# Kernel tuning notes

Measured on AMD Instinct MI355X. Metric: run time of the kernel, lower is better.

## Reference

```python
import jax, jax.numpy as jnp
import numpy as np

N, F, H, C, E = 100000, 128, 64, 16, 1000000


def _prop(x, src, dst, w):
    # gather source features, scale by edge weight, scatter-add to destinations
    msgs = x[src] * w[:, None]  # [E, H]
    return jax.ops.segment_sum(msgs, dst, num_segments=N)


def _gru(x, h, W_ih, W_hh, b_ih, b_hh):
    gi = x @ W_ih.T + b_ih  # [N, 3H]
    gh = h @ W_hh.T + b_hh
    i_r, i_z, i_n = jnp.split(gi, 3, axis=1)
    h_r, h_z, h_n = jnp.split(gh, 3, axis=1)
    r = jax.nn.sigmoid(i_r + h_r)
    z = jax.nn.sigmoid(i_z + h_z)
    n = jnp.tanh(i_n + r * h_n)
    return (1.0 - z) * n + z * h


def setup_inputs() -> dict:
    key = jax.random.key(0)
    ks = jax.random.split(key, 20)
    s = 0.05
    inp = {
        'x': jax.random.normal(ks[0], (N, F), jnp.float32),
        'edge_index': jax.random.randint(ks[1], (2, E), 0, N),
        'edge_weight': jax.random.uniform(ks[2], (E,), jnp.float32),
        'edge_index_re': jax.random.randint(ks[3], (2, E), 0, N),
        'edge_weight_re': jax.random.uniform(ks[4], (E,), jnp.float32),
        'W_first': jax.random.normal(ks[5], (H, F), jnp.float32) * s,
        'b_first': jnp.zeros((H,), jnp.float32),
        'W_con1': jax.random.normal(ks[6], (H, 2 * H), jnp.float32) * s,
        'b_con1': jnp.zeros((H,), jnp.float32),
        'W_con2': jax.random.normal(ks[7], (H, 2 * H), jnp.float32) * s,
        'b_con2': jnp.zeros((H,), jnp.float32),
        'W_lin1': jax.random.normal(ks[8], (H, H), jnp.float32) * s,
        'b_lin1': jnp.zeros((H,), jnp.float32),
        'W_out': jax.random.normal(ks[9], (C, H), jnp.float32) * s,
        'b_out': jnp.zeros((C,), jnp.float32),
        'W_ih': jax.random.normal(ks[10], (3 * H, H), jnp.float32) * s,
        'W_hh': jax.random.normal(ks[11], (3 * H, H), jnp.float32) * s,
        'b_ih': jnp.zeros((3 * H,), jnp.float32),
        'b_hh': jnp.zeros((3 * H,), jnp.float32),
    }
    return inp


def reference(x, edge_index, edge_weight, edge_index_re, edge_weight_re,
              W_first, b_first, W_con1, b_con1, W_con2, b_con2,
              W_lin1, b_lin1, W_out, b_out, W_ih, W_hh, b_ih, b_hh):
    src, dst = edge_index[0], edge_index[1]
    src_r, dst_r = edge_index_re[0], edge_index_re[1]

    x = x @ W_first.T + b_first  # [N, H]; dropout is identity at inference
    h = x

    x1 = _prop(x, src, dst, edge_weight)
    x2 = _prop(x, src_r, dst_r, edge_weight_re)
    x = jnp.concatenate([x1, x2], axis=1) @ W_con1.T + b_con1
    x = _gru(x, h, W_ih, W_hh, b_ih, b_hh)
    x = x @ W_lin1.T + b_lin1

    x1 = _prop(x, src, dst, edge_weight)
    x2 = _prop(x, src_r, dst_r, edge_weight_re)
    x = jnp.concatenate([x1, x2], axis=1) @ W_con2.T + b_con2
    x = _gru(x, h, W_ih, W_hh, b_ih, b_hh)
    x = x @ W_out.T + b_out
    return jax.nn.log_softmax(x, axis=-1)
```

## Files before the change

### kernel.cpp

```cpp
#include <hip/hip_runtime.h>

#define NN 100000
#define FF 128
#define HH 64
#define CC 16
#define EE 1000000
#define NSEG (2*NN)
#define BSH 11
#define BKD  (1 << BSH)
#define NBUK ((NSEG + BKD - 1) / BKD)
#define EPB 4096
#define P1BLK ((2*EE + EPB - 1) / EPB)

typedef __bf16 bf16;
typedef __attribute__((ext_vector_type(8))) __bf16 bf16x8;
typedef __attribute__((ext_vector_type(4))) __bf16 bf16x4;
typedef __attribute__((ext_vector_type(4))) float f32x4;
typedef __attribute__((ext_vector_type(2))) float f32x2;

__device__ __forceinline__ float fsig(float t)  { return 1.0f/(1.0f+__expf(-t)); }
__device__ __forceinline__ float ftanh(float t) { return 1.0f - 2.0f/(__expf(2.0f*t)+1.0f); }

__device__ __forceinline__ unsigned pack_sw(int s, float w) {
    unsigned short u = __builtin_bit_cast(unsigned short, (bf16)w);
    return ((unsigned)s << 15) | (u & 0x7FFFu);
}

__global__ void precomp_kernel(const float* __restrict__ W_ih, const float* __restrict__ b_ih,
                               const float* __restrict__ Wc1,  const float* __restrict__ bc1,
                               const float* __restrict__ Wc2,  const float* __restrict__ bc2,
                               const float* __restrict__ W_hh, const float* __restrict__ W_first,
                               const float* __restrict__ W_lin1, const float* __restrict__ W_out,
                               bf16* __restrict__ W1bf, float* __restrict__ b1,
                               bf16* __restrict__ W2bf, float* __restrict__ b2,
                               bf16* __restrict__ Whbf, bf16* __restrict__ Wfbf,
                               bf16* __restrict__ Wlbf, bf16* __restrict__ Wobf)
{
    int idx = blockIdx.x*blockDim.x + threadIdx.x;
    const int t0 = 192*128;
    const int t1 = t0 + 192;
    const int t2 = t1 + 192*64;
    const int t3 = t2 + 64*128;
    const int t4 = t3 + 64*64;
    const int t5 = t4 + 16*64;
    if (idx < t0) {
        int j = idx >> 7, k = idx & 127;
        float s1 = 0.f, s2 = 0.f;
        for (int m=0; m<64; ++m) {
            float wih = W_ih[j*64+m];
            s1 += wih * Wc1[m*128+k];
            s2 += wih * Wc2[m*128+k];
        }
        W1bf[idx] = (bf16)s1; W2bf[idx] = (bf16)s2;
    } else if (idx < t1) {
        int j = idx - t0;
        float s1 = b_ih[j], s2 = b_ih[j];
        for (int m=0; m<64; ++m) {
            float wih = W_ih[j*64+m];
            s1 += wih * bc1[m];
            s2 += wih * bc2[m];
        }
        b1[j] = s1; b2[j] = s2;
    } else if (idx < t2) {
        int i = idx - t1;  Whbf[i] = (bf16)W_hh[i];
    } else if (idx < t3) {
        int i = idx - t2;  Wfbf[i] = (bf16)W_first[i];
    } else if (idx < t4) {
        int i = idx - t3;  Wlbf[i] = (bf16)W_lin1[i];
    } else if (idx < t5) {
        int i = idx - t4;  Wobf[i] = (bf16)W_out[i];
    }
}


__global__ __launch_bounds__(256) void bucket_count_kernel(const int* __restrict__ ei,
                                                           const int* __restrict__ ei_re,
                                                           int* __restrict__ bkcnt)
{
    __shared__ int hist[NBUK];
    const int t = threadIdx.x;
    for (int i=t; i<NBUK; i+=256) hist[i] = 0;
    __syncthreads();
    const long e0 = (long)blockIdx.x * EPB;
    #pragma unroll
    for (int it=0; it<16; ++it) {
        long e = e0 + it*256 + t;
        int d = -1;
        if (e < EE)        d = ei[EE + e];
        else if (e < 2*EE) d = NN + ei_re[EE + (e - EE)];
        if (d >= 0) atomicAdd(&hist[d >> BSH], 1);
    }
    __syncthreads();
    for (int i=t; i<NBUK; i+=256) if (hist[i]) atomicAdd(&bkcnt[i], hist[i]);
}

__global__ void bucket_scan_kernel(const int* __restrict__ bkcnt,
                                   int* __restrict__ bkbase, int* __restrict__ bkcur,
                                   int* __restrict__ rp)
{
    __shared__ int sc[128];
    const int t = threadIdx.x;
    int v = (t < NBUK) ? bkcnt[t] : 0;
    sc[t] = v;
    __syncthreads();
    #pragma unroll
    for (int off=1; off<128; off<<=1) {
        int x = (t>=off) ? sc[t-off] : 0;
        __syncthreads();
        sc[t] += x;
        __syncthreads();
    }
    int excl = sc[t] - v;
    if (t < NBUK) { bkbase[t] = excl; bkcur[t] = excl; }
    if (t == NBUK-1) bkbase[NBUK] = sc[t];
    if (t == 0) rp[NSEG] = 2*EE;
}

__global__ __launch_bounds__(256) void fillA_kernel(const int* __restrict__ ei,
                                                    const float* __restrict__ ew,
                                                    const int* __restrict__ ei_re,
                                                    const float* __restrict__ ew_re,
                                                    int* __restrict__ bkcur,
                                                    int* __restrict__ tmp_d,
                                                    unsigned* __restrict__ tmp_p)
{
    __shared__ int hist[NBUK];
    __shared__ int base[NBUK];
    const int t = threadIdx.x;
    for (int i=t; i<NBUK; i+=256) hist[i] = 0;
    __syncthreads();
    const long e0 = (long)blockIdx.x * EPB;
    int pr[16];
    #pragma unroll
    for (int it=0; it<16; ++it) {
        long e = e0 + it*256 + t;
        int d = -1;
        if (e < EE)        d = ei[EE + e];
        else if (e < 2*EE) d = NN + ei_re[EE + (e - EE)];
        if (d >= 0) {
            int b = d >> BSH;
            int r = atomicAdd(&hist[b], 1);
            pr[it] = (b << 16) | r;
        } else pr[it] = -1;
    }
    __syncthreads();
    for (int i=t; i<NBUK; i+=256) base[i] = atomicAdd(&bkcur[i], hist[i]);
    __syncthreads();
    #pragma unroll
    for (int it=0; it<16; ++it) {
        if (pr[it] < 0) continue;
        long e = e0 + it*256 + t;
        int d, s; float w;
        if (e < EE) { d = ei[EE+e]; s = ei[e]; w = ew[e]; }
        else { long j = e - EE; d = NN + ei_re[EE+j]; s = ei_re[j]; w = ew_re[j]; }
        int pos = base[pr[it] >> 16] + (pr[it] & 0xFFFF);
        tmp_d[pos] = d;
        tmp_p[pos] = pack_sw(s, w);
    }
}

__global__ __launch_bounds__(1024) void fillB_kernel(const int* __restrict__ bkbase,
                                                     const int* __restrict__ tmp_d,
                                                     const unsigned* __restrict__ tmp_p,
                                                     unsigned* __restrict__ edata,
                                                     int* __restrict__ rp)
{
    __shared__ int cntL[BKD];
    __shared__ int scanL[1024];
    const int t  = threadIdx.x;
    const int b  = blockIdx.x;
    const int d0 = b << BSH;
    const int dn = min(BKD, NSEG - d0);
    const int p0 = bkbase[b];
    const int p1 = bkbase[b+1];
    for (int i=t; i<BKD; i+=1024) cntL[i] = 0;
    __syncthreads();
    for (int pos = p0 + t; pos < p1; pos += 1024)
        atomicAdd(&cntL[tmp_d[pos] - d0], 1);
    __syncthreads();
    int a0 = cntL[2*t], a1 = cntL[2*t+1];
    int ps = a0 + a1;
    scanL[t] = ps;
    __syncthreads();
    #pragma unroll
    for (int off=1; off<1024; off<<=1) {
        int x = (t>=off) ? scanL[t-off] : 0;
        __syncthreads();
        scanL[t] += x;
        __syncthreads();
    }
    int g0 = p0 + scanL[t] - ps;
    int g1 = g0 + a0;
    if (2*t   < dn) rp[d0 + 2*t]   = g0;
    if (2*t+1 < dn) rp[d0 + 2*t+1] = g1;
    cntL[2*t]   = g0;
    cntL[2*t+1] = g1;
    __syncthreads();
    for (int pos = p0 + t; pos < p1; pos += 1024) {
        int d = tmp_d[pos];
        int p = atomicAdd(&cntL[d - d0], 1);
        edata[p] = tmp_p[pos];
    }
}

__global__ __launch_bounds__(256) void csr_prop_kernel(const bf16* __restrict__ X,
    const int* __restrict__ rp, const unsigned* __restrict__ edata,
    bf16* __restrict__ x1, bf16* __restrict__ x2)
{
    int s = blockIdx.x*4 + (threadIdx.x>>6);
    if (s >= NSEG) return;
    const int lane = threadIdx.x & 63;
    const int q  = lane >> 4;
    const int fl = lane & 15;
    const unsigned foff = 8u*(unsigned)fl;
    const int e0 = rp[s], e1 = rp[s+1];
    const char* Xb = (const char*)X;
    const char* Eb = (const char*)edata;

    f32x2 acc01 = {0.f, 0.f}, acc23 = {0.f, 0.f};
    int eq = e0 + q;
    unsigned eqb = 4u*(unsigned)eq;
    for (int base = e0; base < e1; base += 16, eq += 16, eqb += 64u) {
        const int rem = e1 - eq;
        #pragma unroll
        for (int j=0; j<4; ++j) {
            unsigned p = *(const unsigned*)(Eb + (eqb + 16u*(unsigned)j));
            const bool v = (4*j < rem);
            float w = v ? __uint_as_float((p & 0x7FFFu) << 16) : 0.f;
            unsigned voff = v ? (((p >> 8) & 0xFFFFFF80u) | foff) : foff;
            uint2 d = *(const uint2*)(Xb + voff);
            f32x2 lo = { __uint_as_float(d.x << 16), __uint_as_float(d.x & 0xFFFF0000u) };
            f32x2 hi = { __uint_as_float(d.y << 16), __uint_as_float(d.y & 0xFFFF0000u) };
            f32x2 w2 = { w, w };
            acc01 += w2 * lo;
            acc23 += w2 * hi;
        }
    }
    float a0 = acc01.x, a1 = acc01.y, a2 = acc23.x, a3 = acc23.y;
    a0 += __shfl_xor(a0, 32); a0 += __shfl_xor(a0, 16);
    a1 += __shfl_xor(a1, 32); a1 += __shfl_xor(a1, 16);
    a2 += __shfl_xor(a2, 32); a2 += __shfl_xor(a2, 16);
    a3 += __shfl_xor(a3, 32); a3 += __shfl_xor(a3, 16);
    if (q == 0) {
        bf16* o = (s < NN) ? &x1[(long)s*HH] : &x2[(long)(s-NN)*HH];
        bf16x4 ov = {(bf16)a0, (bf16)a1, (bf16)a2, (bf16)a3};
        *(bf16x4*)&o[4*fl] = ov;
    }
}


__global__ __launch_bounds__(256, 2) void lin_first_mfma_kernel(
    const float* __restrict__ X, const bf16* __restrict__ Wf,
    const float* __restrict__ b, float* __restrict__ Y, bf16* __restrict__ Ybf)
{
    const int t = threadIdx.x;
    const int w = t >> 6, lane = t & 63, col = lane & 15, quad = lane >> 4;
    bf16x8 B[4];
    #pragma unroll
    for (int ks=0; ks<4; ++ks)
        B[ks] = *(const bf16x8*)&Wf[(16*w+col)*128 + ks*32 + quad*8];
    const float bv = b[16*w + col];
    __shared__ bf16 Alds[32][136];
    const int m_st = t >> 3, c_in = t & 7;
    for (int tb = blockIdx.x*32; tb < NN; tb += gridDim.x*32) {
        const float4* rx = (const float4*)&X[(long)(tb+m_st)*FF];
        #pragma unroll
        for (int it=0; it<4; ++it) {
            int cc = c_in + it*8;
            float4 v = rx[cc];
            bf16x4 bvv = {(bf16)v.x,(bf16)v.y,(bf16)v.z,(bf16)v.w};
            *(bf16x4*)&Alds[m_st][cc*4] = bvv;
        }
        __syncthreads();
        f32x4 acc[2] = {{0.f,0.f,0.f,0.f},{0.f,0.f,0.f,0.f}};
        #pragma unroll
        for (int ks=0; ks<4; ++ks)
            #pragma unroll
            for (int mt=0; mt<2; ++mt) {
                bf16x8 a = *(const bf16x8*)&Alds[mt*16+col][ks*32+quad*8];
                acc[mt] = __builtin_amdgcn_mfma_f32_16x16x32_bf16(a, B[ks], acc[mt], 0,0,0);
            }
        __syncthreads();
        #pragma unroll
        for (int mt=0; mt<2; ++mt)
            #pragma unroll
            for (int r=0; r<4; ++r) {
                long n = tb + mt*16 + quad*4 + r;
                float val = acc[mt][r] + bv;
                Y  [n*HH + 16*w+col] = val;
                Ybf[n*HH + 16*w+col] = (bf16)val;
            }
    }
}

template<int MODE>
__global__ __launch_bounds__(256, 2) void layer_fused_kernel(
    const bf16* __restrict__ X1, const bf16* __restrict__ X2,
    const float* __restrict__ H, const bf16* __restrict__ Hbf,
    const bf16* __restrict__ Wg, const float* __restrict__ bg,
    const bf16* __restrict__ Wh, const float* __restrict__ bh,
    const bf16* __restrict__ Ws, const float* __restrict__ bs,
    bf16* __restrict__ Obf, float* __restrict__ Of)
{
    const int t    = threadIdx.x;
    const int w    = t >> 6;
    const int lane = t & 63;
    const int col  = lane & 15;
    const int quad = lane >> 4;

    bf16x8 Bg[3][4];
    bf16x8 Bh[3][2];
    float bgv[3], bhv[3];
    #pragma unroll
    for (int jt=0; jt<3; ++jt) {
        int J = jt*64 + 16*w + col;
        #pragma unroll
        for (int ks=0; ks<4; ++ks)
            Bg[jt][ks] = *(const bf16x8*)&Wg[J*128 + ks*32 + quad*8];
        #pragma unroll
        for (int ks=0; ks<2; ++ks)
            Bh[jt][ks] = *(const bf16x8*)&Wh[J*64 + ks*32 + quad*8];
        bgv[jt] = bg[J];
        bhv[jt] = bh[J];
    }

    bf16x8 B2[2];
    float b2s;
    if constexpr (MODE == 0) {
        #pragma unroll
        for (int ks=0; ks<2; ++ks)
            B2[ks] = *(const bf16x8*)&Ws[(16*w+col)*64 + ks*32 + quad*8];
        b2s = bs[16*w + col];
    } else {
        #pragma unroll
        for (int ks=0; ks<2; ++ks)
            B2[ks] = *(const bf16x8*)&Ws[col*64 + ks*32 + quad*8];
        b2s = bs[col];
    }

    __shared__ bf16 Alds[32][200];
    __shared__ bf16 Glds[32][72];

    const int m_st = t >> 3;
    const int c_in = t & 7;

    for (int tb = blockIdx.x*32; tb < NN; tb += gridDim.x*32) {
        {
            long n = tb + m_st;
            *(bf16x8*)&Alds[m_st][c_in*8]       = *(const bf16x8*)&X1[n*HH + c_in*8];
            *(bf16x8*)&Alds[m_st][64 + c_in*8]  = *(const bf16x8*)&X2[n*HH + c_in*8];
            *(bf16x8*)&Alds[m_st][128 + c_in*8] = *(const bf16x8*)&Hbf[n*HH + c_in*8];
        }
        __syncthreads();

        f32x4 accg[2][3];
        f32x4 acch[2][3];
        #pragma unroll
        for (int mt=0; mt<2; ++mt)
            #pragma unroll
            for (int jt=0; jt<3; ++jt) {
                accg[mt][jt] = (f32x4){0.f,0.f,0.f,0.f};
                acch[mt][jt] = (f32x4){0.f,0.f,0.f,0.f};
            }

        #pragma unroll
        for (int ks=0; ks<4; ++ks) {
            #pragma unroll
            for (int mt=0; mt<2; ++mt) {
                bf16x8 a = *(const bf16x8*)&Alds[mt*16 + col][ks*32 + quad*8];
                #pragma unroll
                for (int jt=0; jt<3; ++jt)
                    accg[mt][jt] = __builtin_amdgcn_mfma_f32_16x16x32_bf16(
                        a, Bg[jt][ks], accg[mt][jt], 0, 0, 0);
            }
        }
        #pragma unroll
        for (int ks=0; ks<2; ++ks) {
            #pragma unroll
            for (int mt=0; mt<2; ++mt) {
                bf16x8 a = *(const bf16x8*)&Alds[mt*16 + col][128 + ks*32 + quad*8];
                #pragma unroll
                for (int jt=0; jt<3; ++jt)
                    acch[mt][jt] = __builtin_amdgcn_mfma_f32_16x16x32_bf16(
                        a, Bh[jt][ks], acch[mt][jt], 0, 0, 0);
            }
        }

        const int c = 16*w + col;
        #pragma unroll
        for (int mt=0; mt<2; ++mt) {
            #pragma unroll
            for (int r=0; r<4; ++r) {
                long n = tb + mt*16 + quad*4 + r;
                float gr = accg[mt][0][r] + bgv[0];
                float gz = accg[mt][1][r] + bgv[1];
                float gn = accg[mt][2][r] + bgv[2];
                float hr = acch[mt][0][r] + bhv[0];
                float hz = acch[mt][1][r] + bhv[1];
                float hn = acch[mt][2][r] + bhv[2];
                float rr = fsig(gr + hr);
                float zz = fsig(gz + hz);
                float nv = ftanh(gn + rr*hn);
                float hv = H[n*HH + c];
                Glds[mt*16 + quad*4 + r][c] = (bf16)((1.0f - zz)*nv + zz*hv);
            }
        }
        __syncthreads();

        if constexpr (MODE == 0) {
            f32x4 acc2[2] = {{0.f,0.f,0.f,0.f},{0.f,0.f,0.f,0.f}};
            #pragma unroll
            for (int ks=0; ks<2; ++ks)
                #pragma unroll
                for (int mt=0; mt<2; ++mt) {
                    bf16x8 a = *(const bf16x8*)&Glds[mt*16+col][ks*32+quad*8];
                    acc2[mt] = __builtin_amdgcn_mfma_f32_16x16x32_bf16(a, B2[ks], acc2[mt], 0,0,0);
                }
            #pragma unroll
            for (int mt=0; mt<2; ++mt)
                #pragma unroll
                for (int r=0; r<4; ++r)
                    Obf[(long)(tb+mt*16+quad*4+r)*HH + 16*w+col] = (bf16)(acc2[mt][r] + b2s);
        } else {
            if (w < 2) {
                f32x4 acc2 = {0.f,0.f,0.f,0.f};
                #pragma unroll
                for (int ks=0; ks<2; ++ks) {
                    bf16x8 a = *(const bf16x8*)&Glds[w*16+col][ks*32+quad*8];
                    acc2 = __builtin_amdgcn_mfma_f32_16x16x32_bf16(a, B2[ks], acc2, 0,0,0);
                }
                #pragma unroll
                for (int r=0; r<4; ++r) {
                    long n = tb + w*16 + quad*4 + r;
                    float val = acc2[r] + b2s;
                    float m = val;
                    #pragma unroll
                    for (int off=8; off>0; off>>=1) m = fmaxf(m, __shfl_xor(m, off, 16));
                    float ex = __expf(val - m);
                    float ssum = ex;
                    #pragma unroll
                    for (int off=8; off>0; off>>=1) ssum += __shfl_xor(ssum, off, 16);
                    Of[n*CC + col] = val - m - __logf(ssum);
                }
            }
        }
    }
}

extern "C" void kernel_launch(void* const* d_in, const int* in_sizes, int n_in,
                              void* d_out, int out_size, void* d_ws, size_t ws_size,
                              hipStream_t stream)
{
    const float* x       = (const float*)d_in[0];
    const int*   ei      = (const int*)  d_in[1];
    const float* ew      = (const float*)d_in[2];
    const int*   ei_re   = (const int*)  d_in[3];
    const float* ew_re   = (const float*)d_in[4];
    const float* W_first = (const float*)d_in[5];
    const float* b_first = (const float*)d_in[6];
    const float* W_con1  = (const float*)d_in[7];
    const float* b_con1  = (const float*)d_in[8];
    const float* W_con2  = (const float*)d_in[9];
    const float* b_con2  = (const float*)d_in[10];
    const float* W_lin1  = (const float*)d_in[11];
    const float* b_lin1  = (const float*)d_in[12];
    const float* W_out   = (const float*)d_in[13];
    const float* b_out   = (const float*)d_in[14];
    const float* W_ih    = (const float*)d_in[15];
    const float* W_hh    = (const float*)d_in[16];
    const float* b_ih    = (const float*)d_in[17];
    const float* b_hh    = (const float*)d_in[18];
    float* out = (float*)d_out;

    float* h    = (float*)d_ws;
    bf16*  x1b  = (bf16*)(h + (long)NN*HH);
    bf16*  x2b  = x1b + (long)NN*HH;
    bf16*  hbf  = x2b + (long)NN*HH;
    bf16*  hAbf = hbf + (long)NN*HH;
    float* b1 = (float*)(hAbf + (long)NN*HH);
    float* b2 = b1 + 192;
    bf16*  W1bf = (bf16*)(b2 + 192);
    bf16*  W2bf = W1bf + 192*128;
    bf16*  Whbf = W2bf + 192*128;
    bf16*  Wfbf = Whbf + 192*64;
    bf16*  Wlbf = Wfbf + 64*128;
    bf16*  Wobf = Wlbf + 64*64;
    unsigned* edata = (unsigned*)(Wobf + 16*64);
    int*   rp     = (int*)(edata + 2*EE);
    int*   bkcnt  = rp + NSEG + 1;
    int*   bkbase = bkcnt + NBUK;
    int*   bkcur  = bkbase + NBUK + 1;
    int*      tmp_d = (int*)x1b;
    unsigned* tmp_p = (unsigned*)x2b;

    precomp_kernel<<<(192*128 + 192 + 192*64 + 64*128 + 64*64 + 16*64 + 255)/256, 256, 0, stream>>>(
        W_ih, b_ih, W_con1, b_con1, W_con2, b_con2, W_hh, W_first, W_lin1, W_out,
        W1bf, b1, W2bf, b2, Whbf, Wfbf, Wlbf, Wobf);

    hipMemsetAsync(bkcnt, 0, (size_t)NBUK*sizeof(int), stream);
    bucket_count_kernel<<<P1BLK, 256, 0, stream>>>(ei, ei_re, bkcnt);
    bucket_scan_kernel<<<1, 128, 0, stream>>>(bkcnt, bkbase, bkcur, rp);
    fillA_kernel<<<P1BLK, 256, 0, stream>>>(ei, ew, ei_re, ew_re, bkcur, tmp_d, tmp_p);
    fillB_kernel<<<NBUK, 1024, 0, stream>>>(bkbase, tmp_d, tmp_p, edata, rp);

    lin_first_mfma_kernel<<<1024, 256, 0, stream>>>(x, Wfbf, b_first, h, hbf);

    csr_prop_kernel<<<(NSEG + 3)/4, 256, 0, stream>>>(hbf, rp, edata, x1b, x2b);

    layer_fused_kernel<0><<<1024, 256, 0, stream>>>(x1b, x2b, h, hbf, W1bf, b1, Whbf, b_hh,
                                                    Wlbf, b_lin1, hAbf, nullptr);

    csr_prop_kernel<<<(NSEG + 3)/4, 256, 0, stream>>>(hAbf, rp, edata, x1b, x2b);

    layer_fused_kernel<1><<<1024, 256, 0, stream>>>(x1b, x2b, h, hbf, W2bf, b2, Whbf, b_hh,
                                                    Wobf, b_out, nullptr, out);
}
```

Before: 392.2 us.

## Merge weight precompute into bucket count and first linear into fillB launch

Folds the weight-precompute work into extra blocks of the bucket-count kernel, and runs the first dense projection as extra blocks of the fillB CSR kernel, so independent work shares one launch. This removes two kernel launches and lets the small precompute and the GEMM overlap with the edge-sorting passes. The GEMM blocks now use 1024 threads handling four 32-row tiles each instead of a persistent grid-stride loop, and fillB's shared memory grows to fit the GEMM tiles, which may reduce occupancy.

```diff
diff --git a/kernel.cpp b/kernel.cpp
--- a/kernel.cpp
+++ b/kernel.cpp
@@ -11,6 +11,10 @@
 #define NBUK ((NSEG + BKD - 1) / BKD)
 #define EPB 4096
 #define P1BLK ((2*EE + EPB - 1) / EPB)
+#define PRE_TOT (192*128 + 192 + 192*64 + 64*128 + 64*64 + 16*64)
+#define PRE_BLK ((PRE_TOT + 255)/256)
+#define LIN_TILES ((NN + 31)/32)
+#define LINB ((LIN_TILES + 3)/4)
 
 typedef __bf16 bf16;
 typedef __attribute__((ext_vector_type(8))) __bf16 bf16x8;
@@ -26,7 +30,8 @@
     return ((unsigned)s << 15) | (u & 0x7FFFu);
 }
 
-__global__ void precomp_kernel(const float* __restrict__ W_ih, const float* __restrict__ b_ih,
+__device__ __forceinline__ void precomp_body(int idx,
+                               const float* __restrict__ W_ih, const float* __restrict__ b_ih,
                                const float* __restrict__ Wc1,  const float* __restrict__ bc1,
                                const float* __restrict__ Wc2,  const float* __restrict__ bc2,
                                const float* __restrict__ W_hh, const float* __restrict__ W_first,
@@ -36,7 +41,6 @@
                                bf16* __restrict__ Whbf, bf16* __restrict__ Wfbf,
                                bf16* __restrict__ Wlbf, bf16* __restrict__ Wobf)
 {
-    int idx = blockIdx.x*blockDim.x + threadIdx.x;
     const int t0 = 192*128;
     const int t1 = t0 + 192;
     const int t2 = t1 + 192*64;
@@ -72,26 +76,39 @@
     }
 }
 
-
-__global__ __launch_bounds__(256) void bucket_count_kernel(const int* __restrict__ ei,
-                                                           const int* __restrict__ ei_re,
-                                                           int* __restrict__ bkcnt)
+__global__ __launch_bounds__(256) void count_precomp_kernel(
+    const int* __restrict__ ei, const int* __restrict__ ei_re, int* __restrict__ bkcnt,
+    const float* __restrict__ W_ih, const float* __restrict__ b_ih,
+    const float* __restrict__ Wc1,  const float* __restrict__ bc1,
+    const float* __restrict__ Wc2,  const float* __restrict__ bc2,
+    const float* __restrict__ W_hh, const float* __restrict__ W_first,
+    const float* __restrict__ W_lin1, const float* __restrict__ W_out,
+    bf16* __restrict__ W1bf, float* __restrict__ b1,
+    bf16* __restrict__ W2bf, float* __restrict__ b2,
+    bf16* __restrict__ Whbf, bf16* __restrict__ Wfbf,
+    bf16* __restrict__ Wlbf, bf16* __restrict__ Wobf)
 {
     __shared__ int hist[NBUK];
     const int t = threadIdx.x;
-    for (int i=t; i<NBUK; i+=256) hist[i] = 0;
-    __syncthreads();
-    const long e0 = (long)blockIdx.x * EPB;
-    #pragma unroll
-    for (int it=0; it<16; ++it) {
-        long e = e0 + it*256 + t;
-        int d = -1;
-        if (e < EE)        d = ei[EE + e];
-        else if (e < 2*EE) d = NN + ei_re[EE + (e - EE)];
-        if (d >= 0) atomicAdd(&hist[d >> BSH], 1);
-    }
-    __syncthreads();
-    for (int i=t; i<NBUK; i+=256) if (hist[i]) atomicAdd(&bkcnt[i], hist[i]);
+    if (blockIdx.x < P1BLK) {
+        for (int i=t; i<NBUK; i+=256) hist[i] = 0;
+        __syncthreads();
+        const long e0 = (long)blockIdx.x * EPB;
+        #pragma unroll
+        for (int it=0; it<16; ++it) {
+            long e = e0 + it*256 + t;
+            int d = -1;
+            if (e < EE)        d = ei[EE + e];
+            else if (e < 2*EE) d = NN + ei_re[EE + (e - EE)];
+            if (d >= 0) atomicAdd(&hist[d >> BSH], 1);
+        }
+        __syncthreads();
+        for (int i=t; i<NBUK; i+=256) if (hist[i]) atomicAdd(&bkcnt[i], hist[i]);
+    } else {
+        int idx = (blockIdx.x - P1BLK)*256 + t;
+        precomp_body(idx, W_ih, b_ih, Wc1, bc1, Wc2, bc2, W_hh, W_first, W_lin1, W_out,
+                     W1bf, b1, W2bf, b2, Whbf, Wfbf, Wlbf, Wobf);
+    }
 }
 
 __global__ void bucket_scan_kernel(const int* __restrict__ bkcnt,
@@ -159,47 +176,96 @@
     }
 }
 
-__global__ __launch_bounds__(1024) void fillB_kernel(const int* __restrict__ bkbase,
-                                                     const int* __restrict__ tmp_d,
-                                                     const unsigned* __restrict__ tmp_p,
-                                                     unsigned* __restrict__ edata,
-                                                     int* __restrict__ rp)
-{
-    __shared__ int cntL[BKD];
-    __shared__ int scanL[1024];
-    const int t  = threadIdx.x;
-    const int b  = blockIdx.x;
-    const int d0 = b << BSH;
-    const int dn = min(BKD, NSEG - d0);
-    const int p0 = bkbase[b];
-    const int p1 = bkbase[b+1];
-    for (int i=t; i<BKD; i+=1024) cntL[i] = 0;
-    __syncthreads();
-    for (int pos = p0 + t; pos < p1; pos += 1024)
-        atomicAdd(&cntL[tmp_d[pos] - d0], 1);
-    __syncthreads();
-    int a0 = cntL[2*t], a1 = cntL[2*t+1];
-    int ps = a0 + a1;
-    scanL[t] = ps;
-    __syncthreads();
-    #pragma unroll
-    for (int off=1; off<1024; off<<=1) {
-        int x = (t>=off) ? scanL[t-off] : 0;
-        __syncthreads();
-        scanL[t] += x;
-        __syncthreads();
-    }
-    int g0 = p0 + scanL[t] - ps;
-    int g1 = g0 + a0;
-    if (2*t   < dn) rp[d0 + 2*t]   = g0;
-    if (2*t+1 < dn) rp[d0 + 2*t+1] = g1;
-    cntL[2*t]   = g0;
-    cntL[2*t+1] = g1;
-    __syncthreads();
-    for (int pos = p0 + t; pos < p1; pos += 1024) {
-        int d = tmp_d[pos];
-        int p = atomicAdd(&cntL[d - d0], 1);
-        edata[p] = tmp_p[pos];
+__global__ __launch_bounds__(1024) void fillB_lin_kernel(
+    const int* __restrict__ bkbase,
+    const int* __restrict__ tmp_d, const unsigned* __restrict__ tmp_p,
+    unsigned* __restrict__ edata, int* __restrict__ rp,
+    const float* __restrict__ X, const bf16* __restrict__ Wf,
+    const float* __restrict__ bfirst, float* __restrict__ Y, bf16* __restrict__ Ybf)
+{
+    __shared__ __align__(16) char smem[4*32*136*2];
+    const int t = threadIdx.x;
+    if (blockIdx.x < NBUK) {
+        int* cntL  = (int*)smem;
+        int* scanL = (int*)(smem + BKD*4);
+        const int b  = blockIdx.x;
+        const int d0 = b << BSH;
+        const int dn = min(BKD, NSEG - d0);
+        const int p0 = bkbase[b];
+        const int p1 = bkbase[b+1];
+        for (int i=t; i<BKD; i+=1024) cntL[i] = 0;
+        __syncthreads();
+        for (int pos = p0 + t; pos < p1; pos += 1024)
+            atomicAdd(&cntL[tmp_d[pos] - d0], 1);
+        __syncthreads();
+        int a0 = cntL[2*t], a1 = cntL[2*t+1];
+        int ps = a0 + a1;
+        scanL[t] = ps;
+        __syncthreads();
+        #pragma unroll
+        for (int off=1; off<1024; off<<=1) {
+            int x = (t>=off) ? scanL[t-off] : 0;
+            __syncthreads();
+            scanL[t] += x;
+            __syncthreads();
+        }
+        int g0 = p0 + scanL[t] - ps;
+        int g1 = g0 + a0;
+        if (2*t   < dn) rp[d0 + 2*t]   = g0;
+        if (2*t+1 < dn) rp[d0 + 2*t+1] = g1;
+        cntL[2*t]   = g0;
+        cntL[2*t+1] = g1;
+        __syncthreads();
+        for (int pos = p0 + t; pos < p1; pos += 1024) {
+            int d = tmp_d[pos];
+            int p = atomicAdd(&cntL[d - d0], 1);
+            edata[p] = tmp_p[pos];
+        }
+    } else {
+        const int lb   = blockIdx.x - NBUK;
+        const int sub  = t >> 8;
+        const int tt   = t & 255;
+        const int tile = lb*4 + sub;
+        const bool valid = tile < LIN_TILES;
+        const int tb = tile * 32;
+        const int w = tt >> 6, lane = tt & 63, col = lane & 15, quad = lane >> 4;
+        bf16* Alds = (bf16*)smem + sub*(32*136);
+        bf16x8 B[4];
+        #pragma unroll
+        for (int ks=0; ks<4; ++ks)
+            B[ks] = *(const bf16x8*)&Wf[(16*w+col)*128 + ks*32 + quad*8];
+        const float bv = bfirst[16*w + col];
+        const int m_st = tt >> 3, c_in = tt & 7;
+        if (valid) {
+            const float4* rx = (const float4*)&X[(long)(tb+m_st)*FF];
+            #pragma unroll
+            for (int it=0; it<4; ++it) {
+                int cc = c_in + it*8;
+                float4 v = rx[cc];
+                bf16x4 bvv = {(bf16)v.x,(bf16)v.y,(bf16)v.z,(bf16)v.w};
+                *(bf16x4*)&Alds[m_st*136 + cc*4] = bvv;
+            }
+        }
+        __syncthreads();
+        f32x4 acc[2] = {{0.f,0.f,0.f,0.f},{0.f,0.f,0.f,0.f}};
+        #pragma unroll
+        for (int ks=0; ks<4; ++ks)
+            #pragma unroll
+            for (int mt=0; mt<2; ++mt) {
+                bf16x8 a = *(const bf16x8*)&Alds[(mt*16+col)*136 + ks*32+quad*8];
+                acc[mt] = __builtin_amdgcn_mfma_f32_16x16x32_bf16(a, B[ks], acc[mt], 0,0,0);
+            }
+        if (valid) {
+            #pragma unroll
+            for (int mt=0; mt<2; ++mt)
+                #pragma unroll
+                for (int r=0; r<4; ++r) {
+                    long n = tb + mt*16 + quad*4 + r;
+                    float val = acc[mt][r] + bv;
+                    Y  [n*HH + 16*w+col] = val;
+                    Ybf[n*HH + 16*w+col] = (bf16)val;
+                }
+        }
     }
 }
 
@@ -245,51 +311,6 @@
         bf16* o = (s < NN) ? &x1[(long)s*HH] : &x2[(long)(s-NN)*HH];
         bf16x4 ov = {(bf16)a0, (bf16)a1, (bf16)a2, (bf16)a3};
         *(bf16x4*)&o[4*fl] = ov;
-    }
-}
-
-
-__global__ __launch_bounds__(256, 2) void lin_first_mfma_kernel(
-    const float* __restrict__ X, const bf16* __restrict__ Wf,
-    const float* __restrict__ b, float* __restrict__ Y, bf16* __restrict__ Ybf)
-{
-    const int t = threadIdx.x;
-    const int w = t >> 6, lane = t & 63, col = lane & 15, quad = lane >> 4;
-    bf16x8 B[4];
-    #pragma unroll
-    for (int ks=0; ks<4; ++ks)
-        B[ks] = *(const bf16x8*)&Wf[(16*w+col)*128 + ks*32 + quad*8];
-    const float bv = b[16*w + col];
-    __shared__ bf16 Alds[32][136];
-    const int m_st = t >> 3, c_in = t & 7;
-    for (int tb = blockIdx.x*32; tb < NN; tb += gridDim.x*32) {
-        const float4* rx = (const float4*)&X[(long)(tb+m_st)*FF];
-        #pragma unroll
-        for (int it=0; it<4; ++it) {
-            int cc = c_in + it*8;
-            float4 v = rx[cc];
-            bf16x4 bvv = {(bf16)v.x,(bf16)v.y,(bf16)v.z,(bf16)v.w};
-            *(bf16x4*)&Alds[m_st][cc*4] = bvv;
-        }
-        __syncthreads();
-        f32x4 acc[2] = {{0.f,0.f,0.f,0.f},{0.f,0.f,0.f,0.f}};
-        #pragma unroll
-        for (int ks=0; ks<4; ++ks)
-            #pragma unroll
-            for (int mt=0; mt<2; ++mt) {
-                bf16x8 a = *(const bf16x8*)&Alds[mt*16+col][ks*32+quad*8];
-                acc[mt] = __builtin_amdgcn_mfma_f32_16x16x32_bf16(a, B[ks], acc[mt], 0,0,0);
-            }
-        __syncthreads();
-        #pragma unroll
-        for (int mt=0; mt<2; ++mt)
-            #pragma unroll
-            for (int r=0; r<4; ++r) {
-                long n = tb + mt*16 + quad*4 + r;
-                float val = acc[mt][r] + bv;
-                Y  [n*HH + 16*w+col] = val;
-                Ybf[n*HH + 16*w+col] = (bf16)val;
-            }
     }
 }
 
@@ -493,17 +514,18 @@
     int*      tmp_d = (int*)x1b;
     unsigned* tmp_p = (unsigned*)x2b;
 
-    precomp_kernel<<<(192*128 + 192 + 192*64 + 64*128 + 64*64 + 16*64 + 255)/256, 256, 0, stream>>>(
+    hipMemsetAsync(bkcnt, 0, (size_t)NBUK*sizeof(int), stream);
+    count_precomp_kernel<<<P1BLK + PRE_BLK, 256, 0, stream>>>(
+        ei, ei_re, bkcnt,
         W_ih, b_ih, W_con1, b_con1, W_con2, b_con2, W_hh, W_first, W_lin1, W_out,
         W1bf, b1, W2bf, b2, Whbf, Wfbf, Wlbf, Wobf);
 
-    hipMemsetAsync(bkcnt, 0, (size_t)NBUK*sizeof(int), stream);
-    bucket_count_kernel<<<P1BLK, 256, 0, stream>>>(ei, ei_re, bkcnt);
     bucket_scan_kernel<<<1, 128, 0, stream>>>(bkcnt, bkbase, bkcur, rp);
+
     fillA_kernel<<<P1BLK, 256, 0, stream>>>(ei, ew, ei_re, ew_re, bkcur, tmp_d, tmp_p);
-    fillB_kernel<<<NBUK, 1024, 0, stream>>>(bkbase, tmp_d, tmp_p, edata, rp);
-
-    lin_first_mfma_kernel<<<1024, 256, 0, stream>>>(x, Wfbf, b_first, h, hbf);
+
+    fillB_lin_kernel<<<NBUK + LINB, 1024, 0, stream>>>(
+        bkbase, tmp_d, tmp_p, edata, rp, x, Wfbf, b_first, h, hbf);
 
     csr_prop_kernel<<<(NSEG + 3)/4, 256, 0, stream>>>(hbf, rp, edata, x1b, x2b);
 
```

New measurement: 380.5 us. 1.03x faster.
